# Performance work log

Hardware: AMD Instinct MI355X
Metric: run time of the kernel (lower is better)

Reference implementation:

```python
import jax, jax.numpy as jnp
import numpy as np
import jax.ops

N_NODES = 50000
N_EDGES = 800000
N_GRAPHS = 512
F_IN = 128
HID = 256
N_CLASSES = 1

def _xavier(key, shape):
    fan_in, fan_out = shape[0], shape[1]
    std = (2.0 / (fan_in + fan_out)) ** 0.5
    return jax.random.normal(key, shape, dtype=jnp.float32) * std

def setup_inputs() -> dict:
    key = jax.random.key(0)
    ks = jax.random.split(key, 12)
    x = jax.random.normal(ks[0], (N_NODES, F_IN), dtype=jnp.float32)
    edge_index = jax.random.randint(ks[1], (2, N_EDGES), 0, N_NODES, dtype=jnp.int64)
    batch = jnp.sort(jax.random.randint(ks[2], (N_NODES,), 0, N_GRAPHS, dtype=jnp.int64))
    return {
        'x': x, 'edge_index': edge_index, 'batch': batch,
        'W0': _xavier(ks[3], (F_IN, HID)), 'b0': jnp.zeros((HID,), jnp.float32),
        'W1': _xavier(ks[4], (HID, HID)), 'b1': jnp.zeros((HID,), jnp.float32),
        'W2': _xavier(ks[5], (HID, HID)), 'b2': jnp.zeros((HID,), jnp.float32),
        'Wm1': _xavier(ks[6], (HID, HID)), 'bm1': jnp.zeros((HID,), jnp.float32),
        'Wm2': _xavier(ks[7], (HID, N_CLASSES)), 'bm2': jnp.zeros((N_CLASSES,), jnp.float32),
    }

def _gcn_layer(h, W, b, src, dst, deg_inv_sqrt):
    # PyG GCNConv: linear -> symmetric-normalized aggregation (with self loops) -> bias
    hw = h @ W                                        # [N, out]
    norm = deg_inv_sqrt[src] * deg_inv_sqrt[dst]      # [E]
    msg = hw[src] * norm[:, None]                     # [E, out]
    agg = jax.ops.segment_sum(msg, dst, num_segments=N_NODES)
    agg = agg + hw * (deg_inv_sqrt ** 2)[:, None]     # self-loop term
    return agg + b

def reference(x, edge_index, batch, W0, b0, W1, b1, W2, b2, Wm1, bm1, Wm2, bm2):
    src, dst = edge_index[0], edge_index[1]
    # degree with added self loops (in-degree at dst)
    deg = jax.ops.segment_sum(jnp.ones((N_EDGES,), jnp.float32), dst, num_segments=N_NODES) + 1.0
    deg_inv_sqrt = jax.lax.rsqrt(deg)
    h = jax.nn.relu(_gcn_layer(x, W0, b0, src, dst, deg_inv_sqrt))
    h = jax.nn.relu(_gcn_layer(h, W1, b1, src, dst, deg_inv_sqrt))
    h = jax.nn.relu(_gcn_layer(h, W2, b2, src, dst, deg_inv_sqrt))
    # global mean pool over graphs
    sums = jax.ops.segment_sum(h, batch, num_segments=N_GRAPHS)
    cnts = jax.ops.segment_sum(jnp.ones((N_NODES,), jnp.float32), batch, num_segments=N_GRAPHS)
    pooled = sums / jnp.maximum(cnts, 1.0)[:, None]   # [G, HID]
    out = jax.nn.relu(pooled @ Wm1 + bm1) @ Wm2 + bm2 # [G, num_classes]
    return out
```

## Files before the change

kernel.cpp:

```cpp
#include <hip/hip_runtime.h>

constexpr int N_NODES  = 50000;
constexpr int N_EDGES  = 800000;
constexpr int N_GRAPHS = 512;
constexpr int F_IN     = 128;
constexpr int HID      = 256;
constexpr int NPAD     = 50048;

typedef short short8 __attribute__((ext_vector_type(8)));
typedef float f32x4  __attribute__((ext_vector_type(4)));

__device__ __forceinline__ unsigned short f2b(float f) {
    unsigned u = __float_as_uint(f);
    u += 0x7fffu + ((u >> 16) & 1u);
    return (unsigned short)(u >> 16);
}
__device__ __forceinline__ float b2f_lo(unsigned u) { return __uint_as_float(u << 16); }
__device__ __forceinline__ float b2f_hi(unsigned u) { return __uint_as_float(u & 0xffff0000u); }

__global__ __launch_bounds__(256) void prep_kernel(
    const int* __restrict__ dst, int* __restrict__ deg,
    const float* __restrict__ x, unsigned short* __restrict__ x_bf,
    const float* __restrict__ W0, const float* __restrict__ W1, const float* __restrict__ W2,
    unsigned short* __restrict__ Wt0, unsigned short* __restrict__ Wt1, unsigned short* __restrict__ Wt2)
{
    const int b = blockIdx.x, t = threadIdx.x;
    if (b < 3125) {
        int e = b * 256 + t;
        atomicAdd(&deg[dst[e]], 1);
    } else if (b < 9375) {
        int i = (b - 3125) * 256 + t;
        float4 v = *reinterpret_cast<const float4*>(x + (size_t)i * 4);
        unsigned r0 = (unsigned)f2b(v.x) | ((unsigned)f2b(v.y) << 16);
        unsigned r1 = (unsigned)f2b(v.z) | ((unsigned)f2b(v.w) << 16);
        *reinterpret_cast<uint2*>(x_bf + (size_t)i * 4) = make_uint2(r0, r1);
    } else {
        int i = (b - 9375) * 256 + t;
        const float* W; unsigned short* Wt; int K; int j;
        if (i < 32768)      { W = W0; Wt = Wt0; K = 128; j = i; }
        else if (i < 98304) { W = W1; Wt = Wt1; K = 256; j = i - 32768; }
        else                { W = W2; Wt = Wt2; K = 256; j = i - 98304; }
        int k = j >> 8, n = j & 255;
        int idx = (n >> 7) * (K * 128) + (((k >> 3) * 128 + (n & 127)) << 3) + (k & 7);
        Wt[idx] = f2b(W[j]);
    }
}

__global__ void block_sum_dis_kernel(const int* __restrict__ deg, int* __restrict__ bsum,
                                     float* __restrict__ dis, int n) {
    __shared__ int sm[256];
    int t = threadIdx.x, base = blockIdx.x * 1024;
    int s = 0;
    #pragma unroll
    for (int i = 0; i < 4; ++i) {
        int idx = base + t + i * 256;
        if (idx < n) { int d = deg[idx]; s += d; dis[idx] = rsqrtf((float)d + 1.0f); }
    }
    sm[t] = s; __syncthreads();
    for (int o = 128; o > 0; o >>= 1) { if (t < o) sm[t] += sm[t + o]; __syncthreads(); }
    if (t == 0) bsum[blockIdx.x] = sm[0];
}

__global__ void scan_bsum_kernel(int* __restrict__ bsum, int nb) {
    __shared__ int sm[64];
    int t = threadIdx.x;
    int v = (t < nb) ? bsum[t] : 0;
    sm[t] = v; __syncthreads();
    for (int o = 1; o < 64; o <<= 1) {
        int a = (t >= o) ? sm[t - o] : 0; __syncthreads();
        sm[t] += a; __syncthreads();
    }
    if (t < nb) bsum[t] = sm[t] - v;
}

__global__ void scan_local_kernel(const int* __restrict__ deg, const int* __restrict__ bsum,
                                  int* __restrict__ row_start, int* __restrict__ cursor, int n) {
    __shared__ int sm[256];
    int t = threadIdx.x, base = blockIdx.x * 1024;
    int idx0 = base + t * 4;
    int v[4], s = 0;
    #pragma unroll
    for (int i = 0; i < 4; ++i) { int id = idx0 + i; v[i] = (id < n) ? deg[id] : 0; s += v[i]; }
    sm[t] = s; __syncthreads();
    for (int o = 1; o < 256; o <<= 1) {
        int a = (t >= o) ? sm[t - o] : 0; __syncthreads();
        sm[t] += a; __syncthreads();
    }
    int excl = bsum[blockIdx.x] + sm[t] - s;
    #pragma unroll
    for (int i = 0; i < 4; ++i) {
        int id = idx0 + i;
        if (id < n) { row_start[id] = excl; cursor[id] = excl; }
        excl += v[i];
    }
    if (blockIdx.x == gridDim.x - 1 && t == 255) row_start[n] = excl;
}

__global__ void fill_csr(const int* __restrict__ src, const int* __restrict__ dst,
                         const float* __restrict__ dis, int* __restrict__ cursor,
                         int2* __restrict__ csr) {
    int e = blockIdx.x * blockDim.x + threadIdx.x;
    if (e >= N_EDGES) return;
    int s = src[e], d = dst[e];
    int pos = atomicAdd(&cursor[d], 1);
    float w = dis[s] * dis[d];
    csr[pos] = make_int2(s, __float_as_int(w));
}

template<int F>
__global__ __launch_bounds__(256) void agg_bf16(
    const unsigned short* __restrict__ hin, const int* __restrict__ row_start,
    const int2* __restrict__ csr, const float* __restrict__ dis,
    uint4* __restrict__ out4)
{
    constexpr int LPR  = F / 8;
    constexpr int NSUB = 64 / LPR;
    const int lane = threadIdx.x & 63;
    const int sub  = lane / LPR;
    const int fc   = lane % LPR;
    const int node = blockIdx.x * 4 + (threadIdx.x >> 6);
    if (node >= N_NODES) return;

    float acc[8];
    {
        float dn = dis[node];
        float sw = (sub == 0) ? dn * dn : 0.0f;
        uint2 u2[2];
        *reinterpret_cast<uint4*>(u2) =
            *reinterpret_cast<const uint4*>(hin + (size_t)node * F + fc * 8);
        #pragma unroll
        for (int h = 0; h < 2; ++h) {
            acc[h * 4 + 0] = b2f_lo(u2[h].x) * sw;
            acc[h * 4 + 1] = b2f_hi(u2[h].x) * sw;
            acc[h * 4 + 2] = b2f_lo(u2[h].y) * sw;
            acc[h * 4 + 3] = b2f_hi(u2[h].y) * sw;
        }
    }

    int j = row_start[node] + sub;
    const int end = row_start[node + 1];
    for (; j + 3 * NSUB < end; j += 4 * NSUB) {
        int2 c[4];
        #pragma unroll
        for (int u = 0; u < 4; ++u) c[u] = csr[j + u * NSUB];
        #pragma unroll
        for (int u = 0; u < 4; ++u) {
            float w = __int_as_float(c[u].y);
            uint2 g[2];
            *reinterpret_cast<uint4*>(g) =
                *reinterpret_cast<const uint4*>(hin + (size_t)c[u].x * F + fc * 8);
            #pragma unroll
            for (int h = 0; h < 2; ++h) {
                acc[h * 4 + 0] = fmaf(b2f_lo(g[h].x), w, acc[h * 4 + 0]);
                acc[h * 4 + 1] = fmaf(b2f_hi(g[h].x), w, acc[h * 4 + 1]);
                acc[h * 4 + 2] = fmaf(b2f_lo(g[h].y), w, acc[h * 4 + 2]);
                acc[h * 4 + 3] = fmaf(b2f_hi(g[h].y), w, acc[h * 4 + 3]);
            }
        }
    }
    for (; j < end; j += NSUB) {
        int2 c0 = csr[j];
        float w = __int_as_float(c0.y);
        uint2 g[2];
        *reinterpret_cast<uint4*>(g) =
            *reinterpret_cast<const uint4*>(hin + (size_t)c0.x * F + fc * 8);
        #pragma unroll
        for (int h = 0; h < 2; ++h) {
            acc[h * 4 + 0] = fmaf(b2f_lo(g[h].x), w, acc[h * 4 + 0]);
            acc[h * 4 + 1] = fmaf(b2f_hi(g[h].x), w, acc[h * 4 + 1]);
            acc[h * 4 + 2] = fmaf(b2f_lo(g[h].y), w, acc[h * 4 + 2]);
            acc[h * 4 + 3] = fmaf(b2f_hi(g[h].y), w, acc[h * 4 + 3]);
        }
    }

    #pragma unroll
    for (int k = 0; k < 8; ++k) {
        #pragma unroll
        for (int off = LPR; off < 64; off <<= 1)
            acc[k] += __shfl_xor(acc[k], off, 64);
    }

    if (sub == 0) {
        uint2 r[2];
        #pragma unroll
        for (int h = 0; h < 2; ++h) {
            r[h].x = (unsigned)f2b(acc[h * 4 + 0]) | ((unsigned)f2b(acc[h * 4 + 1]) << 16);
            r[h].y = (unsigned)f2b(acc[h * 4 + 2]) | ((unsigned)f2b(acc[h * 4 + 3]) << 16);
        }
        int chunk = (node >> 7) * (128 * (F / 8)) + fc * 128 + (node & 127);
        out4[chunk] = *reinterpret_cast<uint4*>(r);
    }
}

template<int K>
__global__ __launch_bounds__(256) void gemm_frag(
    const uint4* __restrict__ A4,
    const unsigned short* __restrict__ Wt_frag,
    const float* __restrict__ bias,
    unsigned short* __restrict__ C,
    int relu)
{
    __shared__ __align__(16) unsigned short Bs[K * 128];
    const int t    = threadIdx.x;
    const int lane = t & 63;
    const int w    = t >> 6;
    const int wm   = w & 1, wn = w >> 1;
    const int q    = lane >> 4, m = lane & 15;
    const int panel = blockIdx.x;
    const int col0  = blockIdx.y * 128;

    {
        const uint4* src4 = reinterpret_cast<const uint4*>(Wt_frag + blockIdx.y * (K * 128));
        uint4* dst4 = reinterpret_cast<uint4*>(Bs);
        #pragma unroll
        for (int it = 0; it < K / 16; ++it)
            dst4[it * 256 + t] = src4[it * 256 + t];
    }
    __syncthreads();

    f32x4 acc[4][4] = {};
    const int abase = panel * (128 * (K / 8));

    #pragma unroll
    for (int kb = 0; kb < K / 32; ++kb) {
        short8 af[4], bf[4];
        #pragma unroll
        for (int i = 0; i < 4; ++i) {
            uint4 v = A4[abase + (kb * 4 + q) * 128 + wm * 64 + i * 16 + m];
            af[i] = *reinterpret_cast<short8*>(&v);
        }
        #pragma unroll
        for (int jn = 0; jn < 4; ++jn)
            bf[jn] = *reinterpret_cast<const short8*>(&Bs[((kb * 4 + q) * 128 + wn * 64 + jn * 16 + m) * 8]);
        #pragma unroll
        for (int i = 0; i < 4; ++i)
            #pragma unroll
            for (int jn = 0; jn < 4; ++jn)
                acc[i][jn] = __builtin_amdgcn_mfma_f32_16x16x32_bf16(af[i], bf[jn], acc[i][jn], 0, 0, 0);
    }

    #pragma unroll
    for (int jn = 0; jn < 4; ++jn) {
        int col = col0 + wn * 64 + jn * 16 + m;
        float bj = bias[col];
        #pragma unroll
        for (int i = 0; i < 4; ++i) {
            int rowb = panel * 128 + wm * 64 + i * 16 + q * 4;
            #pragma unroll
            for (int r = 0; r < 4; ++r) {
                float v = acc[i][jn][r] + bj;
                if (relu) v = fmaxf(v, 0.f);
                C[(size_t)(rowb + r) * 256 + col] = f2b(v);
            }
        }
    }
}

__global__ __launch_bounds__(256) void pool_mlp_kernel(
    const unsigned short* __restrict__ h, const int* __restrict__ batch,
    const float* __restrict__ Wm1, const float* __restrict__ bm1,
    const float* __restrict__ Wm2, const float* __restrict__ bm2,
    float* __restrict__ out)
{
    __shared__ float p[HID];
    __shared__ float red[HID];
    __shared__ int se[2];
    const int g = blockIdx.x, t = threadIdx.x;
    if (t < 2) {
        int target = g + t;
        int lo = 0, hi = N_NODES;
        while (lo < hi) { int mid = (lo + hi) >> 1; if (batch[mid] < target) lo = mid + 1; else hi = mid; }
        se[t] = lo;
    }
    __syncthreads();
    const int s = se[0], e = se[1];
    float acc = 0.f;
    for (int n = s; n < e; ++n) acc += b2f_lo((unsigned)h[(size_t)n * HID + t]);
    p[t] = acc / fmaxf((float)(e - s), 1.0f);
    __syncthreads();
    float a2 = bm1[t];
    for (int k = 0; k < HID; ++k) a2 = fmaf(p[k], Wm1[k * HID + t], a2);
    red[t] = fmaxf(a2, 0.f) * Wm2[t];
    __syncthreads();
    for (int o = 128; o > 0; o >>= 1) {
        if (t < o) red[t] += red[t + o];
        __syncthreads();
    }
    if (t == 0) out[g] = red[0] + bm2[0];
}

extern "C" void kernel_launch(void* const* d_in, const int* in_sizes, int n_in,
                              void* d_out, int out_size, void* d_ws, size_t ws_size,
                              hipStream_t stream) {
    const float* x    = (const float*)d_in[0];
    const int*   ei   = (const int*)d_in[1];
    const int*   batch= (const int*)d_in[2];
    const float* W0   = (const float*)d_in[3];
    const float* b0   = (const float*)d_in[4];
    const float* W1   = (const float*)d_in[5];
    const float* b1   = (const float*)d_in[6];
    const float* W2   = (const float*)d_in[7];
    const float* b2   = (const float*)d_in[8];
    const float* Wm1  = (const float*)d_in[9];
    const float* bm1  = (const float*)d_in[10];
    const float* Wm2  = (const float*)d_in[11];
    const float* bm2  = (const float*)d_in[12];
    float* out = (float*)d_out;

    char* ws = (char*)d_ws;
    size_t off = 0;
    auto alloc = [&](size_t bytes) -> void* {
        void* p = ws + off;
        off += (bytes + 255) & ~(size_t)255;
        return p;
    };
    int*   deg       = (int*)  alloc((size_t)N_NODES * 4);
    float* dis       = (float*)alloc((size_t)N_NODES * 4);
    int*   row_start = (int*)  alloc((size_t)(N_NODES + 1) * 4);
    int*   cursor    = (int*)  alloc((size_t)N_NODES * 4);
    int*   bsum      = (int*)  alloc((size_t)64 * 4);
    int2*  csr       = (int2*) alloc((size_t)N_EDGES * 8);
    unsigned short* x_bf = (unsigned short*)alloc((size_t)N_NODES * F_IN * 2);
    unsigned short* Wt0  = (unsigned short*)alloc((size_t)F_IN * HID * 2);
    unsigned short* Wt1  = (unsigned short*)alloc((size_t)HID * HID * 2);
    unsigned short* Wt2  = (unsigned short*)alloc((size_t)HID * HID * 2);
    unsigned short* bufA = (unsigned short*)alloc((size_t)NPAD * HID * 2);
    unsigned short* bufB = (unsigned short*)alloc((size_t)NPAD * HID * 2);

    const int* src = ei;
    const int* dst = ei + N_EDGES;
    const int NB = (N_NODES + 1023) / 1024;

    hipMemsetAsync(deg, 0, (size_t)N_NODES * 4, stream);
    prep_kernel         <<<10015, 256, 0, stream>>>(dst, deg, x, x_bf, W0, W1, W2, Wt0, Wt1, Wt2);
    block_sum_dis_kernel<<<NB, 256, 0, stream>>>(deg, bsum, dis, N_NODES);
    scan_bsum_kernel    <<<1, 64, 0, stream>>>(bsum, NB);
    scan_local_kernel   <<<NB, 256, 0, stream>>>(deg, bsum, row_start, cursor, N_NODES);
    fill_csr            <<<(N_EDGES + 255) / 256, 256, 0, stream>>>(src, dst, dis, cursor, csr);

    dim3 ggrid(NPAD / 128, 2);

    agg_bf16<F_IN><<<(N_NODES + 3) / 4, 256, 0, stream>>>(x_bf, row_start, csr, dis, (uint4*)bufA);
    gemm_frag<F_IN><<<ggrid, 256, 0, stream>>>((const uint4*)bufA, Wt0, b0, bufB, 1);

    agg_bf16<HID><<<(N_NODES + 3) / 4, 256, 0, stream>>>(bufB, row_start, csr, dis, (uint4*)bufA);
    gemm_frag<HID><<<ggrid, 256, 0, stream>>>((const uint4*)bufA, Wt1, b1, bufB, 1);

    agg_bf16<HID><<<(N_NODES + 3) / 4, 256, 0, stream>>>(bufB, row_start, csr, dis, (uint4*)bufA);
    gemm_frag<HID><<<ggrid, 256, 0, stream>>>((const uint4*)bufA, Wt2, b2, bufB, 1);

    pool_mlp_kernel<<<N_GRAPHS, HID, 0, stream>>>(bufB, batch, Wm1, bm1, Wm2, bm2, out);
}
```

Before: 430.2 us.

## Chunk feature layout by 32 columns and compress CSR to 16-bit source indices

Stores node features in a column-chunked layout (32 bf16 per node per chunk) and schedules aggregation blocks per chunk so each chunk's gather working set can fit in L2. The CSR shrinks to 16-bit source indices, with edge weights recomputed from dis at gather time instead of stored. Aggregation uses 4 lanes per node per chunk with no cross-lane reduction, and GEMM output and pooling are updated to the new layout. Risks are the extra dis gather per edge and load imbalance from varying node degrees within a wave.

```diff
diff --git a/kernel.cpp b/kernel.cpp
--- a/kernel.cpp
+++ b/kernel.cpp
@@ -9,6 +9,7 @@
 
 typedef short short8 __attribute__((ext_vector_type(8)));
 typedef float f32x4  __attribute__((ext_vector_type(4)));
+typedef unsigned int u32x4 __attribute__((ext_vector_type(4)));
 
 __device__ __forceinline__ unsigned short f2b(float f) {
     unsigned u = __float_as_uint(f);
@@ -33,7 +34,9 @@
         float4 v = *reinterpret_cast<const float4*>(x + (size_t)i * 4);
         unsigned r0 = (unsigned)f2b(v.x) | ((unsigned)f2b(v.y) << 16);
         unsigned r1 = (unsigned)f2b(v.z) | ((unsigned)f2b(v.w) << 16);
-        *reinterpret_cast<uint2*>(x_bf + (size_t)i * 4) = make_uint2(r0, r1);
+        int node = i >> 5, c = (i & 31) >> 3, slot = i & 7;
+        *reinterpret_cast<uint2*>(x_bf + (((size_t)c * NPAD + node) << 5) + slot * 4) =
+            make_uint2(r0, r1);
     } else {
         int i = (b - 9375) * 256 + t;
         const float* W; unsigned short* Wt; int K; int j;
@@ -97,99 +100,84 @@
 }
 
 __global__ void fill_csr(const int* __restrict__ src, const int* __restrict__ dst,
-                         const float* __restrict__ dis, int* __restrict__ cursor,
-                         int2* __restrict__ csr) {
+                         int* __restrict__ cursor, unsigned short* __restrict__ csr16) {
     int e = blockIdx.x * blockDim.x + threadIdx.x;
     if (e >= N_EDGES) return;
-    int s = src[e], d = dst[e];
+    int d = dst[e];
     int pos = atomicAdd(&cursor[d], 1);
-    float w = dis[s] * dis[d];
-    csr[pos] = make_int2(s, __float_as_int(w));
+    csr16[pos] = (unsigned short)src[e];
+}
+
+__device__ __forceinline__ void fma8(float* acc, uint4 g, float wt) {
+    acc[0] = fmaf(b2f_lo(g.x), wt, acc[0]); acc[1] = fmaf(b2f_hi(g.x), wt, acc[1]);
+    acc[2] = fmaf(b2f_lo(g.y), wt, acc[2]); acc[3] = fmaf(b2f_hi(g.y), wt, acc[3]);
+    acc[4] = fmaf(b2f_lo(g.z), wt, acc[4]); acc[5] = fmaf(b2f_hi(g.z), wt, acc[5]);
+    acc[6] = fmaf(b2f_lo(g.w), wt, acc[6]); acc[7] = fmaf(b2f_hi(g.w), wt, acc[7]);
 }
 
 template<int F>
-__global__ __launch_bounds__(256) void agg_bf16(
-    const unsigned short* __restrict__ hin, const int* __restrict__ row_start,
-    const int2* __restrict__ csr, const float* __restrict__ dis,
+__global__ __launch_bounds__(256) void agg_chunked(
+    const unsigned short* __restrict__ hin,
+    const int* __restrict__ row_start,
+    const unsigned short* __restrict__ csr_src,
+    const float* __restrict__ dis,
     uint4* __restrict__ out4)
 {
-    constexpr int LPR  = F / 8;
-    constexpr int NSUB = 64 / LPR;
-    const int lane = threadIdx.x & 63;
-    const int sub  = lane / LPR;
-    const int fc   = lane % LPR;
-    const int node = blockIdx.x * 4 + (threadIdx.x >> 6);
+    const int gid = blockIdx.x;
+    int chunk, nb;
+    if (F == 256) {
+        chunk = gid & 7; nb = gid >> 3;
+    } else {
+        int s = gid & 7; chunk = s & 3; nb = (s >> 2) * 391 + (gid >> 3);
+    }
+    const int t    = threadIdx.x;
+    const int node = nb * 64 + (t >> 2);
+    const int fl   = t & 3;
     if (node >= N_NODES) return;
 
+    const uint4* hc = reinterpret_cast<const uint4*>(hin) + (size_t)chunk * (NPAD * 4);
+
+    const float dn = dis[node];
     float acc[8];
     {
-        float dn = dis[node];
-        float sw = (sub == 0) ? dn * dn : 0.0f;
-        uint2 u2[2];
-        *reinterpret_cast<uint4*>(u2) =
-            *reinterpret_cast<const uint4*>(hin + (size_t)node * F + fc * 8);
-        #pragma unroll
-        for (int h = 0; h < 2; ++h) {
-            acc[h * 4 + 0] = b2f_lo(u2[h].x) * sw;
-            acc[h * 4 + 1] = b2f_hi(u2[h].x) * sw;
-            acc[h * 4 + 2] = b2f_lo(u2[h].y) * sw;
-            acc[h * 4 + 3] = b2f_hi(u2[h].y) * sw;
-        }
-    }
-
-    int j = row_start[node] + sub;
+        uint4 sv = hc[(node << 2) + fl];
+        float sw = dn * dn;
+        acc[0] = b2f_lo(sv.x) * sw; acc[1] = b2f_hi(sv.x) * sw;
+        acc[2] = b2f_lo(sv.y) * sw; acc[3] = b2f_hi(sv.y) * sw;
+        acc[4] = b2f_lo(sv.z) * sw; acc[5] = b2f_hi(sv.z) * sw;
+        acc[6] = b2f_lo(sv.w) * sw; acc[7] = b2f_hi(sv.w) * sw;
+    }
+
+    int j = row_start[node];
     const int end = row_start[node + 1];
-    for (; j + 3 * NSUB < end; j += 4 * NSUB) {
-        int2 c[4];
-        #pragma unroll
-        for (int u = 0; u < 4; ++u) c[u] = csr[j + u * NSUB];
-        #pragma unroll
-        for (int u = 0; u < 4; ++u) {
-            float w = __int_as_float(c[u].y);
-            uint2 g[2];
-            *reinterpret_cast<uint4*>(g) =
-                *reinterpret_cast<const uint4*>(hin + (size_t)c[u].x * F + fc * 8);
-            #pragma unroll
-            for (int h = 0; h < 2; ++h) {
-                acc[h * 4 + 0] = fmaf(b2f_lo(g[h].x), w, acc[h * 4 + 0]);
-                acc[h * 4 + 1] = fmaf(b2f_hi(g[h].x), w, acc[h * 4 + 1]);
-                acc[h * 4 + 2] = fmaf(b2f_lo(g[h].y), w, acc[h * 4 + 2]);
-                acc[h * 4 + 3] = fmaf(b2f_hi(g[h].y), w, acc[h * 4 + 3]);
-            }
-        }
-    }
-    for (; j < end; j += NSUB) {
-        int2 c0 = csr[j];
-        float w = __int_as_float(c0.y);
-        uint2 g[2];
-        *reinterpret_cast<uint4*>(g) =
-            *reinterpret_cast<const uint4*>(hin + (size_t)c0.x * F + fc * 8);
-        #pragma unroll
-        for (int h = 0; h < 2; ++h) {
-            acc[h * 4 + 0] = fmaf(b2f_lo(g[h].x), w, acc[h * 4 + 0]);
-            acc[h * 4 + 1] = fmaf(b2f_hi(g[h].x), w, acc[h * 4 + 1]);
-            acc[h * 4 + 2] = fmaf(b2f_lo(g[h].y), w, acc[h * 4 + 2]);
-            acc[h * 4 + 3] = fmaf(b2f_hi(g[h].y), w, acc[h * 4 + 3]);
-        }
-    }
-
-    #pragma unroll
-    for (int k = 0; k < 8; ++k) {
-        #pragma unroll
-        for (int off = LPR; off < 64; off <<= 1)
-            acc[k] += __shfl_xor(acc[k], off, 64);
-    }
-
-    if (sub == 0) {
-        uint2 r[2];
-        #pragma unroll
-        for (int h = 0; h < 2; ++h) {
-            r[h].x = (unsigned)f2b(acc[h * 4 + 0]) | ((unsigned)f2b(acc[h * 4 + 1]) << 16);
-            r[h].y = (unsigned)f2b(acc[h * 4 + 2]) | ((unsigned)f2b(acc[h * 4 + 3]) << 16);
-        }
-        int chunk = (node >> 7) * (128 * (F / 8)) + fc * 128 + (node & 127);
-        out4[chunk] = *reinterpret_cast<uint4*>(r);
-    }
+    for (; j + 4 <= end; j += 4) {
+        int s0 = __builtin_nontemporal_load(&csr_src[j + 0]);
+        int s1 = __builtin_nontemporal_load(&csr_src[j + 1]);
+        int s2 = __builtin_nontemporal_load(&csr_src[j + 2]);
+        int s3 = __builtin_nontemporal_load(&csr_src[j + 3]);
+        uint4 g0 = hc[(s0 << 2) + fl];
+        uint4 g1 = hc[(s1 << 2) + fl];
+        uint4 g2 = hc[(s2 << 2) + fl];
+        uint4 g3 = hc[(s3 << 2) + fl];
+        float w0 = dis[s0] * dn, w1 = dis[s1] * dn, w2 = dis[s2] * dn, w3 = dis[s3] * dn;
+        fma8(acc, g0, w0); fma8(acc, g1, w1); fma8(acc, g2, w2); fma8(acc, g3, w3);
+    }
+    for (; j < end; ++j) {
+        int s0 = __builtin_nontemporal_load(&csr_src[j]);
+        uint4 g0 = hc[(s0 << 2) + fl];
+        float w0 = dis[s0] * dn;
+        fma8(acc, g0, w0);
+    }
+
+    u32x4 r;
+    r.x = (unsigned)f2b(acc[0]) | ((unsigned)f2b(acc[1]) << 16);
+    r.y = (unsigned)f2b(acc[2]) | ((unsigned)f2b(acc[3]) << 16);
+    r.z = (unsigned)f2b(acc[4]) | ((unsigned)f2b(acc[5]) << 16);
+    r.w = (unsigned)f2b(acc[6]) | ((unsigned)f2b(acc[7]) << 16);
+    const int fcg = chunk * 4 + fl;
+    __builtin_nontemporal_store(
+        r, reinterpret_cast<u32x4*>(
+               &out4[(size_t)(node >> 7) * (128 * (F / 8)) + fcg * 128 + (node & 127)]));
 }
 
 template<int K>
@@ -243,6 +231,7 @@
     for (int jn = 0; jn < 4; ++jn) {
         int col = col0 + wn * 64 + jn * 16 + m;
         float bj = bias[col];
+        int cch = col >> 5, o = col & 31;
         #pragma unroll
         for (int i = 0; i < 4; ++i) {
             int rowb = panel * 128 + wm * 64 + i * 16 + q * 4;
@@ -250,7 +239,7 @@
             for (int r = 0; r < 4; ++r) {
                 float v = acc[i][jn][r] + bj;
                 if (relu) v = fmaxf(v, 0.f);
-                C[(size_t)(rowb + r) * 256 + col] = f2b(v);
+                C[((size_t)cch * NPAD + (rowb + r)) * 32 + o] = f2b(v);
             }
         }
     }
@@ -274,8 +263,9 @@
     }
     __syncthreads();
     const int s = se[0], e = se[1];
+    const size_t cbase = (size_t)(t >> 5) * NPAD * 32 + (t & 31);
     float acc = 0.f;
-    for (int n = s; n < e; ++n) acc += b2f_lo((unsigned)h[(size_t)n * HID + t]);
+    for (int n = s; n < e; ++n) acc += b2f_lo((unsigned)h[cbase + (size_t)n * 32]);
     p[t] = acc / fmaxf((float)(e - s), 1.0f);
     __syncthreads();
     float a2 = bm1[t];
@@ -319,13 +309,13 @@
     int*   row_start = (int*)  alloc((size_t)(N_NODES + 1) * 4);
     int*   cursor    = (int*)  alloc((size_t)N_NODES * 4);
     int*   bsum      = (int*)  alloc((size_t)64 * 4);
-    int2*  csr       = (int2*) alloc((size_t)N_EDGES * 8);
-    unsigned short* x_bf = (unsigned short*)alloc((size_t)N_NODES * F_IN * 2);
-    unsigned short* Wt0  = (unsigned short*)alloc((size_t)F_IN * HID * 2);
-    unsigned short* Wt1  = (unsigned short*)alloc((size_t)HID * HID * 2);
-    unsigned short* Wt2  = (unsigned short*)alloc((size_t)HID * HID * 2);
-    unsigned short* bufA = (unsigned short*)alloc((size_t)NPAD * HID * 2);
-    unsigned short* bufB = (unsigned short*)alloc((size_t)NPAD * HID * 2);
+    unsigned short* csr16 = (unsigned short*)alloc((size_t)N_EDGES * 2);
+    unsigned short* x_bf  = (unsigned short*)alloc((size_t)NPAD * F_IN * 2);
+    unsigned short* Wt0   = (unsigned short*)alloc((size_t)F_IN * HID * 2);
+    unsigned short* Wt1   = (unsigned short*)alloc((size_t)HID * HID * 2);
+    unsigned short* Wt2   = (unsigned short*)alloc((size_t)HID * HID * 2);
+    unsigned short* bufA  = (unsigned short*)alloc((size_t)NPAD * HID * 2);
+    unsigned short* bufB  = (unsigned short*)alloc((size_t)NPAD * HID * 2);
 
     const int* src = ei;
     const int* dst = ei + N_EDGES;
@@ -336,17 +326,17 @@
     block_sum_dis_kernel<<<NB, 256, 0, stream>>>(deg, bsum, dis, N_NODES);
     scan_bsum_kernel    <<<1, 64, 0, stream>>>(bsum, NB);
     scan_local_kernel   <<<NB, 256, 0, stream>>>(deg, bsum, row_start, cursor, N_NODES);
-    fill_csr            <<<(N_EDGES + 255) / 256, 256, 0, stream>>>(src, dst, dis, cursor, csr);
+    fill_csr            <<<(N_EDGES + 255) / 256, 256, 0, stream>>>(src, dst, cursor, csr16);
 
     dim3 ggrid(NPAD / 128, 2);
 
-    agg_bf16<F_IN><<<(N_NODES + 3) / 4, 256, 0, stream>>>(x_bf, row_start, csr, dis, (uint4*)bufA);
+    agg_chunked<F_IN><<<391 * 8, 256, 0, stream>>>(x_bf, row_start, csr16, dis, (uint4*)bufA);
     gemm_frag<F_IN><<<ggrid, 256, 0, stream>>>((const uint4*)bufA, Wt0, b0, bufB, 1);
 
-    agg_bf16<HID><<<(N_NODES + 3) / 4, 256, 0, stream>>>(bufB, row_start, csr, dis, (uint4*)bufA);
+    agg_chunked<HID><<<782 * 8, 256, 0, stream>>>(bufB, row_start, csr16, dis, (uint4*)bufA);
     gemm_frag<HID><<<ggrid, 256, 0, stream>>>((const uint4*)bufA, Wt1, b1, bufB, 1);
 
-    agg_bf16<HID><<<(N_NODES + 3) / 4, 256, 0, stream>>>(bufB, row_start, csr, dis, (uint4*)bufA);
+    agg_chunked<HID><<<782 * 8, 256, 0, stream>>>(bufB, row_start, csr16, dis, (uint4*)bufA);
     gemm_frag<HID><<<ggrid, 256, 0, stream>>>((const uint4*)bufA, Wt2, b2, bufB, 1);
 
     pool_mlp_kernel<<<N_GRAPHS, HID, 0, stream>>>(bufB, batch, Wm1, bm1, Wm2, bm2, out);
```

Measured after the change: 502.1 us. 16.7% more time.
